# Optimization experiments

Hardware: AMD Instinct MI355X
Metric: run time of the kernel (lower is better)

Reference implementation:

```python
import jax, jax.numpy as jnp
import numpy as np

N = 100000   # nodes per graph-set
E = 600000   # edges
G = 64       # graphs in batch
H = 128      # hidden size (atom_h == voro_h == embeddings)
STEPS = 4
F_B = 90     # atom feature length
F_V = 20     # voro feature length


def setup_inputs() -> dict:
    key = jax.random.key(0)
    ks = jax.random.split(key, 16)
    inp = {
        "x_b": jax.random.uniform(ks[0], (N, F_B), dtype=jnp.float32),
        "edge_index_b": jax.random.randint(ks[1], (2, E), 0, N, dtype=jnp.int32),
        "batch_b": jnp.sort(jax.random.randint(ks[2], (N,), 0, G, dtype=jnp.int32)),
        "x_v": jax.random.uniform(ks[3], (N, F_V), dtype=jnp.float32),
        "edge_index_v": jax.random.randint(ks[4], (2, E), 0, N, dtype=jnp.int32),
        "batch_v": jnp.sort(jax.random.randint(ks[5], (N,), 0, G, dtype=jnp.int32)),
        # embedding linears (bias=False)
        "W_emb_b": jax.random.normal(ks[6], (F_B, H), dtype=jnp.float32) * 0.05,
        "W_emb_v": jax.random.normal(ks[7], (F_V, H), dtype=jnp.float32) * 0.05,
        # GatedGraphConv (the *bond* block — source applies it to both graphs)
        "ggc_weight": jax.random.normal(ks[8], (STEPS, H, H), dtype=jnp.float32) * 0.05,
        "gru_w_ih": jax.random.normal(ks[9], (3 * H, H), dtype=jnp.float32) * 0.05,
        "gru_w_hh": jax.random.normal(ks[10], (3 * H, H), dtype=jnp.float32) * 0.05,
        "gru_b_ih": jnp.zeros((3 * H,), dtype=jnp.float32),
        "gru_b_hh": jnp.zeros((3 * H,), dtype=jnp.float32),
        # output block (hidden = 2H)
        "W1": jax.random.normal(ks[11], (2 * H, 2 * H), dtype=jnp.float32) * 0.05,
        "b1": jnp.zeros((2 * H,), dtype=jnp.float32),
        "W2": jax.random.normal(ks[12], (2 * H, 1), dtype=jnp.float32) * 0.05,
        "b2": jnp.zeros((1,), dtype=jnp.float32),
    }
    return inp


def _gru_cell(m, h, w_ih, w_hh, b_ih, b_hh):
    gi = m @ w_ih.T + b_ih   # [N, 3H]
    gh = h @ w_hh.T + b_hh
    i_r, i_z, i_n = jnp.split(gi, 3, axis=-1)
    h_r, h_z, h_n = jnp.split(gh, 3, axis=-1)
    r = jax.nn.sigmoid(i_r + h_r)
    z = jax.nn.sigmoid(i_z + h_z)
    n = jnp.tanh(i_n + r * h_n)
    return (1.0 - z) * n + z * h


def _gated_graph_conv(x, edge_index, ggc_weight, gru_w_ih, gru_w_hh, gru_b_ih, gru_b_hh):
    # x: [N, H] (in_channels == out_channels, no padding needed)
    src, dst = edge_index[0], edge_index[1]
    h = x
    for i in range(STEPS):
        m = h @ ggc_weight[i]                                   # [N, H]
        agg = jax.ops.segment_sum(m[src], dst, num_segments=N)  # add-aggregation
        h = _gru_cell(agg, h, gru_w_ih, gru_w_hh, gru_b_ih, gru_b_hh)
    return h


def _mean_pool(x, batch):
    sums = jax.ops.segment_sum(x, batch, num_segments=G)
    cnt = jax.ops.segment_sum(jnp.ones((x.shape[0],), x.dtype), batch, num_segments=G)
    return sums / jnp.maximum(cnt, 1.0)[:, None]


def reference(x_b, edge_index_b, batch_b, x_v, edge_index_v, batch_v,
              W_emb_b, W_emb_v, ggc_weight, gru_w_ih, gru_w_hh, gru_b_ih, gru_b_hh,
              W1, b1, W2, b2):
    # embedding blocks: relu(linear(x)) (no bias)
    hb = jax.nn.relu(x_b @ W_emb_b)
    hv = jax.nn.relu(x_v @ W_emb_v)
    # NOTE: source (faithfully) applies mpnn_layer_bond to BOTH graphs
    hb = _gated_graph_conv(hb, edge_index_b, ggc_weight, gru_w_ih, gru_w_hh, gru_b_ih, gru_b_hh)
    hv = _gated_graph_conv(hv, edge_index_v, ggc_weight, gru_w_ih, gru_w_hh, gru_b_ih, gru_b_hh)
    gb = _mean_pool(jax.nn.relu(hb), batch_b)   # [G, H]
    gv = _mean_pool(jax.nn.relu(hv), batch_v)   # [G, H]
    g = jnp.concatenate([gb, gv], axis=1)       # [G, 2H]
    out = jax.nn.softplus(jax.nn.relu(g @ W1 + b1) @ W2 + b2)
    return out.squeeze(1)                       # [G]
```

## Files before the change

kernel.cpp:

```cpp
#include <hip/hip_runtime.h>
#include <hip/hip_bf16.h>
#include <math.h>

#define N_NODES   100000
#define N_EDGES   600000
#define NG        64
#define H         128
#define STEPS     4
#define FB        90
#define FV        20
#define NN        (2*N_NODES)
#define EE        (2*N_EDGES)
#define BSTR      40
#define NBLK      196
#define NNP       (NBLK*1024)

#define WCAT_KC   (12*64*8)
#define WCAT_HALF (8*WCAT_KC)
#define WCAT_STEP (2*WCAT_HALF)

typedef unsigned short u16;
typedef __attribute__((ext_vector_type(8))) __bf16 bf16x8;
typedef __attribute__((ext_vector_type(4))) float  floatx4;

static __device__ __forceinline__ float bf16_lo(unsigned u){ return __uint_as_float(u << 16); }
static __device__ __forceinline__ float bf16_hi(unsigned u){ return __uint_as_float(u & 0xffff0000u); }
static __device__ __forceinline__ u16 f2bf(float f){
    union { float f; unsigned u; } v; v.f = f;
    unsigned r = v.u + 0x7fffu + ((v.u >> 16) & 1u);
    return (u16)(r >> 16);
}
static __device__ __forceinline__ float fastrcp(float x){ return __builtin_amdgcn_rcpf(x); }
static __device__ __forceinline__ float fsigmoid(float x){ return fastrcp(1.f + __expf(-x)); }
static __device__ __forceinline__ float ftanh(float x){ return 1.f - 2.f*fastrcp(1.f + __expf(2.f*x)); }


__global__ void deg_kernel(const int* __restrict__ eib, const int* __restrict__ eiv,
                           int* __restrict__ deg){
    int e = blockIdx.x*blockDim.x + threadIdx.x;
    if (e >= EE) return;
    int d;
    if (e < N_EDGES) d = eib[N_EDGES + e];
    else             d = eiv[N_EDGES + (e - N_EDGES)] + N_NODES;
    atomicAdd(&deg[d], 1);
}

__global__ __launch_bounds__(256) void bsum_kernel(const int* __restrict__ deg, int* __restrict__ bsum){
    int t = threadIdx.x;
    int4 v = reinterpret_cast<const int4*>(deg)[blockIdx.x*256 + t];
    int s = v.x + v.y + v.z + v.w;
    __shared__ int ss[256];
    ss[t] = s; __syncthreads();
    for (int off = 128; off > 0; off >>= 1){ if (t < off) ss[t] += ss[t + off]; __syncthreads(); }
    if (t == 0) bsum[blockIdx.x] = ss[0];
}

__global__ __launch_bounds__(256) void bscan_kernel(const int* __restrict__ bsum, int* __restrict__ boff){
    int t = threadIdx.x;
    int v = (t < NBLK) ? bsum[t] : 0;
    __shared__ int ss[256];
    ss[t] = v; __syncthreads();
    for (int off = 1; off < 256; off <<= 1){
        int u = (t >= off) ? ss[t - off] : 0;
        __syncthreads();
        ss[t] += u;
        __syncthreads();
    }
    boff[t] = ss[t] - v;
}

__global__ __launch_bounds__(256) void scan_final_kernel(const int* __restrict__ deg, const int* __restrict__ boff,
                                                         int* __restrict__ row_ptr, int* __restrict__ cursor){
    int t = threadIdx.x, b = blockIdx.x;
    int4 v = reinterpret_cast<const int4*>(deg)[b*256 + t];
    int s = v.x + v.y + v.z + v.w;
    __shared__ int ss[256];
    ss[t] = s; __syncthreads();
    for (int off = 1; off < 256; off <<= 1){
        int u = (t >= off) ? ss[t - off] : 0;
        __syncthreads();
        ss[t] += u;
        __syncthreads();
    }
    int base = boff[b] + ss[t] - s;
    int i0 = b*1024 + t*4;
    int e0 = base, e1 = e0 + v.x, e2 = e1 + v.y, e3 = e2 + v.z;
    if (i0 < NN){
        int4 w = make_int4(e0, e1, e2, e3);
        reinterpret_cast<int4*>(row_ptr)[i0 >> 2] = w;
        reinterpret_cast<int4*>(cursor)[i0 >> 2]  = w;
    }
    if (b == 0 && t == 0) row_ptr[NN] = EE;
}

__global__ void csr_fill_kernel(const int* __restrict__ eib, const int* __restrict__ eiv,
                                int* __restrict__ cursor, int* __restrict__ csr_src){
    int e = blockIdx.x*blockDim.x + threadIdx.x;
    if (e >= EE) return;
    int s, d;
    if (e < N_EDGES){ s = eib[e];                 d = eib[N_EDGES + e]; }
    else { int e2 = e - N_EDGES; s = eiv[e2] + N_NODES; d = eiv[N_EDGES + e2] + N_NODES; }
    int pos = atomicAdd(&cursor[d], 1);
    csr_src[pos] = s;
}

__global__ __launch_bounds__(128) void fold_kernel(const float* __restrict__ ggc_w,
                                                   const float* __restrict__ w_ih,
                                                   float* __restrict__ Bfold){
    int blk = blockIdx.x;
    int s = blk >> 7, k = blk & 127;
    __shared__ float wg[128];
    int t = threadIdx.x;
    wg[t] = ggc_w[(size_t)s*H*H + (size_t)k*H + t];
    __syncthreads();
    for (int c = t; c < 384; c += 128){
        const float* wr = w_ih + (size_t)c*H;
        float acc = 0.f;
        for (int q = 0; q < 128; q += 4){
            float4 a = *reinterpret_cast<const float4*>(&wg[q]);
            float4 b = *reinterpret_cast<const float4*>(&wr[q]);
            acc += a.x*b.x + a.y*b.y + a.z*b.z + a.w*b.w;
        }
        Bfold[((size_t)s*H + k)*384 + c] = acc;
    }
}

__global__ void pack_kernel(const float* __restrict__ Bfold, const float* __restrict__ w_hh,
                            u16* __restrict__ Wcat){
    int idx = blockIdx.x*256 + threadIdx.x;
    if (idx >= STEPS*WCAT_STEP) return;
    int v    = idx & 7;
    int lane = (idx >> 3) & 63;
    int t    = (idx >> 9) % 12;
    int rem  = idx / (512*12);
    int kc   = rem & 7;
    int b1   = (rem >> 3) & 1;
    int s    = rem >> 4;
    int col16 = lane & 15, l4 = lane >> 4;
    int k = kc*32 + l4*8 + v;
    int g = t >> 2, jj = t & 3;
    int c = (4*b1 + jj)*16 + col16;
    int gc = (g == 2) ? (256 + c) : (g*128 + c);
    float val;
    if (k < 128) val = Bfold[((size_t)s*H + k)*384 + gc];
    else         val = w_hh[(size_t)gc*H + (k - 128)];
    Wcat[idx] = f2bf(val);
}


__global__ __launch_bounds__(128) void emb_kernel(const float* __restrict__ xb, const float* __restrict__ xv,
                                                  const float* __restrict__ Wb, const float* __restrict__ Wv,
                                                  u16* __restrict__ hb){
    __shared__ float xs[8][FB];
    int j = threadIdx.x;
    int n0 = blockIdx.x * 8;
    const float* x; const float* W; int K; int xoff;
    if (n0 < N_NODES){ x = xb; W = Wb; K = FB; xoff = n0; }
    else             { x = xv; W = Wv; K = FV; xoff = n0 - N_NODES; }
    for (int i = j; i < 8*K; i += 128){ int r = i / K, c = i - r*K; xs[r][c] = x[(xoff + r)*K + c]; }
    __syncthreads();
    float acc[8];
    #pragma unroll
    for (int n = 0; n < 8; ++n) acc[n] = 0.f;
    for (int k = 0; k < K; ++k){
        float w = W[k*H + j];
        #pragma unroll
        for (int n = 0; n < 8; ++n) acc[n] = fmaf(xs[n][k], w, acc[n]);
    }
    #pragma unroll
    for (int n = 0; n < 8; ++n)
        hb[(size_t)(n0 + n)*H + j] = f2bf(fmaxf(acc[n], 0.f));
}


__global__ __launch_bounds__(256) void agg_kernel(const u16* __restrict__ hb,
                                                  const int* __restrict__ row_ptr,
                                                  const int* __restrict__ csr_src,
                                                  u16* __restrict__ aggb){
    int wid  = threadIdx.x >> 6;
    int lane = threadIdx.x & 63;
    int half = lane >> 5;
    int c    = lane & 31;
    int node = blockIdx.x*4 + wid;
    int beg = row_ptr[node], end = row_ptr[node+1];
    const uint2* rows = reinterpret_cast<const uint2*>(hb);
    float s0 = 0.f, s1 = 0.f, s2 = 0.f, s3 = 0.f;
    float t0 = 0.f, t1 = 0.f, t2 = 0.f, t3 = 0.f;
    int e = beg + half;
    for (; e + 2 < end; e += 4){
        int sA = csr_src[e];
        int sB = csr_src[e + 2];
        uint2 uA = rows[(size_t)sA*32 + c];
        uint2 uB = rows[(size_t)sB*32 + c];
        s0 += bf16_lo(uA.x); s1 += bf16_hi(uA.x); s2 += bf16_lo(uA.y); s3 += bf16_hi(uA.y);
        t0 += bf16_lo(uB.x); t1 += bf16_hi(uB.x); t2 += bf16_lo(uB.y); t3 += bf16_hi(uB.y);
    }
    if (e < end){
        int sA = csr_src[e];
        uint2 uA = rows[(size_t)sA*32 + c];
        s0 += bf16_lo(uA.x); s1 += bf16_hi(uA.x); s2 += bf16_lo(uA.y); s3 += bf16_hi(uA.y);
    }
    s0 += t0; s1 += t1; s2 += t2; s3 += t3;
    s0 += __shfl_xor(s0, 32); s1 += __shfl_xor(s1, 32);
    s2 += __shfl_xor(s2, 32); s3 += __shfl_xor(s3, 32);
    if (half == 0){
        uint2 o;
        o.x = (unsigned)f2bf(s0) | ((unsigned)f2bf(s1) << 16);
        o.y = (unsigned)f2bf(s2) | ((unsigned)f2bf(s3) << 16);
        reinterpret_cast<uint2*>(aggb)[(size_t)node*32 + c] = o;
    }
}


__global__ __launch_bounds__(256, 3) void gru_mfma_kernel(const u16* __restrict__ aggb,
                                                          const u16* __restrict__ hb_in,
                                                          u16* __restrict__ hb_out,
                                                          const u16* __restrict__ Wcat,
                                                          const float* __restrict__ b_ih,
                                                          const float* __restrict__ b_hh){
    __shared__ u16 Bs[WCAT_KC];
    __shared__ u16 As[64*BSTR];
    const int t = threadIdx.x;
    const int wid = t >> 6, lane = t & 63;
    const int l15 = lane & 15, l4 = lane >> 4;
    const int n0 = blockIdx.x * 64;
    const int b1 = blockIdx.y;
    const u16* Wsrc = Wcat + (size_t)b1*WCAT_HALF;

    floatx4 accR[4], accZ[4], accNi[4], accNh[4];
    #pragma unroll
    for (int i = 0; i < 4; ++i){
        accR[i] = (floatx4){0.f,0.f,0.f,0.f};  accZ[i]  = (floatx4){0.f,0.f,0.f,0.f};
        accNi[i] = (floatx4){0.f,0.f,0.f,0.f}; accNh[i] = (floatx4){0.f,0.f,0.f,0.f};
    }

    for (int kc = 0; kc < 8; ++kc){
        __syncthreads();
        {
            const u16* src = Wsrc + (size_t)kc*WCAT_KC;
            #pragma unroll
            for (int p = 0; p < 3; ++p){
                int i = t + p*256;
                *reinterpret_cast<int4*>(&Bs[i*8]) = *reinterpret_cast<const int4*>(src + (size_t)i*8);
            }
        }
        {
            int row = t >> 2, part = t & 3;
            const u16* srcA = (kc < 4) ? aggb : hb_in;
            const int4 v = *reinterpret_cast<const int4*>(srcA + (size_t)(n0 + row)*H + (kc & 3)*32 + part*8);
            *reinterpret_cast<int4*>(&As[row*BSTR + part*8]) = v;
        }
        __syncthreads();
        bf16x8 aF = *reinterpret_cast<const bf16x8*>(&As[(wid*16 + l15)*BSTR + l4*8]);
        if (kc < 4){
            #pragma unroll
            for (int j = 0; j < 4; ++j){
                bf16x8 bR = *reinterpret_cast<const bf16x8*>(&Bs[((0*4 + j)*64 + lane)*8]);
                bf16x8 bZ = *reinterpret_cast<const bf16x8*>(&Bs[((1*4 + j)*64 + lane)*8]);
                bf16x8 bN = *reinterpret_cast<const bf16x8*>(&Bs[((2*4 + j)*64 + lane)*8]);
                accR[j]  = __builtin_amdgcn_mfma_f32_16x16x32_bf16(aF, bR, accR[j], 0, 0, 0);
                accZ[j]  = __builtin_amdgcn_mfma_f32_16x16x32_bf16(aF, bZ, accZ[j], 0, 0, 0);
                accNi[j] = __builtin_amdgcn_mfma_f32_16x16x32_bf16(aF, bN, accNi[j], 0, 0, 0);
            }
        } else {
            #pragma unroll
            for (int j = 0; j < 4; ++j){
                bf16x8 bR = *reinterpret_cast<const bf16x8*>(&Bs[((0*4 + j)*64 + lane)*8]);
                bf16x8 bZ = *reinterpret_cast<const bf16x8*>(&Bs[((1*4 + j)*64 + lane)*8]);
                bf16x8 bN = *reinterpret_cast<const bf16x8*>(&Bs[((2*4 + j)*64 + lane)*8]);
                accR[j]  = __builtin_amdgcn_mfma_f32_16x16x32_bf16(aF, bR, accR[j], 0, 0, 0);
                accZ[j]  = __builtin_amdgcn_mfma_f32_16x16x32_bf16(aF, bZ, accZ[j], 0, 0, 0);
                accNh[j] = __builtin_amdgcn_mfma_f32_16x16x32_bf16(aF, bN, accNh[j], 0, 0, 0);
            }
        }
    }

    const int rowb = n0 + wid*16 + l4*4;
    #pragma unroll
    for (int jj = 0; jj < 4; ++jj){
        int col = (4*b1 + jj)*16 + l15;
        float br  = b_ih[col]       + b_hh[col];
        float bz  = b_ih[128 + col] + b_hh[128 + col];
        float bin = b_ih[256 + col];
        float bhn = b_hh[256 + col];
        #pragma unroll
        for (int rg = 0; rg < 4; ++rg){
            int row = rowb + rg;
            float r   = fsigmoid(accR[jj][rg] + br);
            float z   = fsigmoid(accZ[jj][rg] + bz);
            float nn_ = ftanh(accNi[jj][rg] + bin + r*(accNh[jj][rg] + bhn));
            float hold = bf16_lo((unsigned)hb_in[(size_t)row*H + col]);
            float hnew = (1.f - z)*nn_ + z*hold;
            hb_out[(size_t)row*H + col] = f2bf(hnew);
        }
    }
}


__global__ __launch_bounds__(128) void pool_kernel(const u16* __restrict__ hb,
                                                   const int* __restrict__ batch_b, const int* __restrict__ batch_v,
                                                   float* __restrict__ pool){
    int j  = threadIdx.x;
    int n0 = blockIdx.x * 32;
    bool voro = (n0 >= N_NODES);
    int colbase = voro ? 128 : 0;
    int gcur = -1; float acc = 0.f;
    for (int r = 0; r < 32; ++r){
        int node = n0 + r;
        int g = voro ? batch_v[node - N_NODES] : batch_b[node];
        if (g != gcur){
            if (gcur >= 0) atomicAdd(&pool[gcur*256 + colbase + j], acc);
            acc = 0.f; gcur = g;
        }
        acc += fmaxf(bf16_lo((unsigned)hb[(size_t)node*H + j]), 0.f);
    }
    if (gcur >= 0) atomicAdd(&pool[gcur*256 + colbase + j], acc);
}

__global__ __launch_bounds__(256) void cnt_kernel(const int* __restrict__ batch_b, const int* __restrict__ batch_v,
                                                  int* __restrict__ cnt){
    __shared__ int bins[128];
    int t = threadIdx.x;
    if (t < 128) bins[t] = 0;
    __syncthreads();
    int i = blockIdx.x*256 + t;
    if (i < NN){
        int g = (i < N_NODES) ? batch_b[i] : 64 + batch_v[i - N_NODES];
        atomicAdd(&bins[g], 1);
    }
    __syncthreads();
    if (t < 128 && bins[t] > 0) atomicAdd(&cnt[t], bins[t]);
}


__global__ __launch_bounds__(256) void head_kernel(const float* __restrict__ pool, const int* __restrict__ cnt,
                                                   const float* __restrict__ W1, const float* __restrict__ b1,
                                                   const float* __restrict__ W2, const float* __restrict__ b2,
                                                   float* __restrict__ out){
    __shared__ float gs[256];
    __shared__ float wsum[4];
    int b = blockIdx.x, j = threadIdx.x;
    int c = (j < 128) ? cnt[b] : cnt[64 + b];
    float denom = (float)((c > 1) ? c : 1);
    gs[j] = pool[b*256 + j] / denom;
    __syncthreads();
    float acc = b1[j];
    for (int k = 0; k < 256; ++k) acc = fmaf(gs[k], W1[k*256 + j], acc);
    float y = fmaxf(acc, 0.f) * W2[j];
    #pragma unroll
    for (int off = 32; off > 0; off >>= 1) y += __shfl_down(y, off, 64);
    if ((j & 63) == 0) wsum[j >> 6] = y;
    __syncthreads();
    if (j == 0){
        float x = wsum[0] + wsum[1] + wsum[2] + wsum[3] + b2[0];
        float sp = (x > 0.f) ? x + log1pf(expf(-x)) : log1pf(expf(x));
        out[b] = sp;
    }
}


extern "C" void kernel_launch(void* const* d_in, const int* in_sizes, int n_in,
                              void* d_out, int out_size, void* d_ws, size_t ws_size,
                              hipStream_t stream){
    const float* x_b      = (const float*)d_in[0];
    const int*   eib      = (const int*)  d_in[1];
    const int*   batch_b  = (const int*)  d_in[2];
    const float* x_v      = (const float*)d_in[3];
    const int*   eiv      = (const int*)  d_in[4];
    const int*   batch_v  = (const int*)  d_in[5];
    const float* W_emb_b  = (const float*)d_in[6];
    const float* W_emb_v  = (const float*)d_in[7];
    const float* ggc_w    = (const float*)d_in[8];
    const float* gru_w_ih = (const float*)d_in[9];
    const float* gru_w_hh = (const float*)d_in[10];
    const float* gru_b_ih = (const float*)d_in[11];
    const float* gru_b_hh = (const float*)d_in[12];
    const float* W1       = (const float*)d_in[13];
    const float* b1       = (const float*)d_in[14];
    const float* W2       = (const float*)d_in[15];
    const float* b2       = (const float*)d_in[16];
    float* out = (float*)d_out;

    char* ws = (char*)d_ws;
    size_t off = 0;
    auto alloc = [&](size_t bytes)->char*{
        char* p = ws + off; off += (bytes + 255)/256*256; return p;
    };
    u16*   hb0      = (u16*)   alloc((size_t)NN*H*2);
    u16*   hb1      = (u16*)   alloc((size_t)NN*H*2);
    u16*   aggb     = (u16*)   alloc((size_t)NN*H*2);
    float* Bfold    = (float*) alloc((size_t)STEPS*H*384*4);
    u16*   Wcat     = (u16*)   alloc((size_t)STEPS*WCAT_STEP*2);
    int*   row_ptr  = (int*)   alloc((size_t)(NN+1)*4);
    int*   deg      = (int*)   alloc((size_t)NNP*4);
    int*   cursor   = (int*)   alloc((size_t)NN*4);
    int*   csr_src  = (int*)   alloc((size_t)EE*4);
    int*   bsum     = (int*)   alloc((size_t)256*4);
    int*   boff     = (int*)   alloc((size_t)256*4);
    float* pool     = (float*) alloc((size_t)NG*2*H*4);
    int*   cnt      = (int*)   alloc((size_t)2*NG*4);
    (void)ws_size; (void)in_sizes; (void)n_in; (void)out_size;

    hipMemsetAsync(deg,  0, (size_t)NNP*4, stream);
    hipMemsetAsync(pool, 0, (size_t)NG*2*H*4, stream);
    hipMemsetAsync(cnt,  0, (size_t)2*NG*4, stream);

    deg_kernel        <<<(EE + 255)/256, 256, 0, stream>>>(eib, eiv, deg);
    bsum_kernel       <<<NBLK, 256, 0, stream>>>(deg, bsum);
    bscan_kernel      <<<1, 256, 0, stream>>>(bsum, boff);
    scan_final_kernel <<<NBLK, 256, 0, stream>>>(deg, boff, row_ptr, cursor);
    csr_fill_kernel   <<<(EE + 255)/256, 256, 0, stream>>>(eib, eiv, cursor, csr_src);
    fold_kernel       <<<STEPS*H, 128, 0, stream>>>(ggc_w, gru_w_ih, Bfold);
    pack_kernel       <<<(STEPS*WCAT_STEP + 255)/256, 256, 0, stream>>>(Bfold, gru_w_hh, Wcat);

    emb_kernel<<<NN/8, 128, 0, stream>>>(x_b, x_v, W_emb_b, W_emb_v, hb0);

    u16* hbs[2] = { hb0, hb1 };
    for (int s = 0; s < STEPS; ++s){
        u16* hin  = hbs[s & 1];
        u16* hout = hbs[(s + 1) & 1];
        agg_kernel     <<<NN/4, 256, 0, stream>>>(hin, row_ptr, csr_src, aggb);
        gru_mfma_kernel<<<dim3(NN/64, 2), 256, 0, stream>>>(aggb, hin, hout,
                                                            Wcat + (size_t)s*WCAT_STEP,
                                                            gru_b_ih, gru_b_hh);
    }

    pool_kernel<<<NN/32, 128, 0, stream>>>(hb0, batch_b, batch_v, pool);
    cnt_kernel <<<(NN + 255)/256, 256, 0, stream>>>(batch_b, batch_v, cnt);
    head_kernel<<<NG, 256, 0, stream>>>(pool, cnt, W1, b1, W2, b2, out);
}
```

Measured before the change: 937.1 us.

## Build CSR via two-level bucket sort and widen aggregation gathers to 16 bytes

Replaces the single-pass atomic CSR fill with a two-stage bucketed sort. Edges are first appended into 64-node buckets using per-bucket global atomics, with the blocks partitioned by bucket group. Each bucket is then scattered into csr_src using shared-memory atomics, aiming to cut contended global atomics and make the scattered writes more local. Separately, the aggregation kernel now gathers 16-byte rows with four edge lanes per node instead of two, which needs an extra shuffle-reduction stage; the new CSR build also adds two kernels and an extra buffer.

```diff
diff --git a/kernel.cpp b/kernel.cpp
--- a/kernel.cpp
+++ b/kernel.cpp
@@ -14,6 +14,7 @@
 #define BSTR      40
 #define NBLK      196
 #define NNP       (NBLK*1024)
+#define NBUCK     (NN/64)
 
 #define WCAT_KC   (12*64*8)
 #define WCAT_HALF (8*WCAT_KC)
@@ -70,7 +71,7 @@
 }
 
 __global__ __launch_bounds__(256) void scan_final_kernel(const int* __restrict__ deg, const int* __restrict__ boff,
-                                                         int* __restrict__ row_ptr, int* __restrict__ cursor){
+                                                         int* __restrict__ row_ptr){
     int t = threadIdx.x, b = blockIdx.x;
     int4 v = reinterpret_cast<const int4*>(deg)[b*256 + t];
     int s = v.x + v.y + v.z + v.w;
@@ -86,22 +87,48 @@
     int i0 = b*1024 + t*4;
     int e0 = base, e1 = e0 + v.x, e2 = e1 + v.y, e3 = e2 + v.z;
     if (i0 < NN){
-        int4 w = make_int4(e0, e1, e2, e3);
-        reinterpret_cast<int4*>(row_ptr)[i0 >> 2] = w;
-        reinterpret_cast<int4*>(cursor)[i0 >> 2]  = w;
+        reinterpret_cast<int4*>(row_ptr)[i0 >> 2] = make_int4(e0, e1, e2, e3);
     }
     if (b == 0 && t == 0) row_ptr[NN] = EE;
 }
 
-__global__ void csr_fill_kernel(const int* __restrict__ eib, const int* __restrict__ eiv,
-                                int* __restrict__ cursor, int* __restrict__ csr_src){
-    int e = blockIdx.x*blockDim.x + threadIdx.x;
-    if (e >= EE) return;
-    int s, d;
-    if (e < N_EDGES){ s = eib[e];                 d = eib[N_EDGES + e]; }
-    else { int e2 = e - N_EDGES; s = eiv[e2] + N_NODES; d = eiv[N_EDGES + e2] + N_NODES; }
-    int pos = atomicAdd(&cursor[d], 1);
-    csr_src[pos] = s;
+__global__ void bcur_init_kernel(const int* __restrict__ row_ptr, int* __restrict__ bcur){
+    int b = blockIdx.x*blockDim.x + threadIdx.x;
+    if (b < NBUCK) bcur[b] = row_ptr[b*64];
+}
+
+__global__ __launch_bounds__(256) void bucket_fill_kernel(const int* __restrict__ eib, const int* __restrict__ eiv,
+                                                          int* __restrict__ bcur, int* __restrict__ bucket_buf){
+    int g   = blockIdx.x & 7;
+    int bid = blockIdx.x >> 3;
+    int nb  = gridDim.x >> 3;
+    for (int e = bid*256 + threadIdx.x; e < EE; e += nb*256){
+        int s, d;
+        if (e < N_EDGES){ s = eib[e];                 d = eib[N_EDGES + e]; }
+        else { int e2 = e - N_EDGES; s = eiv[e2] + N_NODES; d = eiv[N_EDGES + e2] + N_NODES; }
+        int b = d >> 6;
+        if ((b & 7) == g){
+            int pos = atomicAdd(&bcur[b], 1);
+            bucket_buf[pos] = (s << 6) | (d & 63);
+        }
+    }
+}
+
+__global__ __launch_bounds__(256) void bucket_scatter_kernel(const int* __restrict__ bucket_buf,
+                                                             const int* __restrict__ row_ptr,
+                                                             int* __restrict__ csr_src){
+    __shared__ int cur[64];
+    int b = blockIdx.x, t = threadIdx.x;
+    int base = row_ptr[b*64];
+    int cnt  = row_ptr[b*64 + 64] - base;
+    if (t < 64) cur[t] = row_ptr[b*64 + t];
+    __syncthreads();
+    for (int i = t; i < cnt; i += 256){
+        int entry = bucket_buf[base + i];
+        int d = entry & 63, s = entry >> 6;
+        int pos = atomicAdd(&cur[d], 1);
+        csr_src[pos] = s;
+    }
 }
 
 __global__ __launch_bounds__(128) void fold_kernel(const float* __restrict__ ggc_w,
@@ -179,35 +206,42 @@
                                                   u16* __restrict__ aggb){
     int wid  = threadIdx.x >> 6;
     int lane = threadIdx.x & 63;
-    int half = lane >> 5;
-    int c    = lane & 31;
+    int q    = lane >> 4;
+    int c    = lane & 15;
     int node = blockIdx.x*4 + wid;
     int beg = row_ptr[node], end = row_ptr[node+1];
-    const uint2* rows = reinterpret_cast<const uint2*>(hb);
-    float s0 = 0.f, s1 = 0.f, s2 = 0.f, s3 = 0.f;
-    float t0 = 0.f, t1 = 0.f, t2 = 0.f, t3 = 0.f;
-    int e = beg + half;
-    for (; e + 2 < end; e += 4){
+    const uint4* rows = reinterpret_cast<const uint4*>(hb);
+    float s0=0.f,s1=0.f,s2=0.f,s3=0.f,s4=0.f,s5=0.f,s6=0.f,s7=0.f;
+    float u0=0.f,u1=0.f,u2=0.f,u3=0.f,u4=0.f,u5=0.f,u6=0.f,u7=0.f;
+    int e = beg + q;
+    for (; e + 4 < end; e += 8){
         int sA = csr_src[e];
-        int sB = csr_src[e + 2];
-        uint2 uA = rows[(size_t)sA*32 + c];
-        uint2 uB = rows[(size_t)sB*32 + c];
-        s0 += bf16_lo(uA.x); s1 += bf16_hi(uA.x); s2 += bf16_lo(uA.y); s3 += bf16_hi(uA.y);
-        t0 += bf16_lo(uB.x); t1 += bf16_hi(uB.x); t2 += bf16_lo(uB.y); t3 += bf16_hi(uB.y);
+        int sB = csr_src[e + 4];
+        uint4 a = rows[(size_t)sA*16 + c];
+        uint4 b = rows[(size_t)sB*16 + c];
+        s0 += bf16_lo(a.x); s1 += bf16_hi(a.x); s2 += bf16_lo(a.y); s3 += bf16_hi(a.y);
+        s4 += bf16_lo(a.z); s5 += bf16_hi(a.z); s6 += bf16_lo(a.w); s7 += bf16_hi(a.w);
+        u0 += bf16_lo(b.x); u1 += bf16_hi(b.x); u2 += bf16_lo(b.y); u3 += bf16_hi(b.y);
+        u4 += bf16_lo(b.z); u5 += bf16_hi(b.z); u6 += bf16_lo(b.w); u7 += bf16_hi(b.w);
     }
     if (e < end){
         int sA = csr_src[e];
-        uint2 uA = rows[(size_t)sA*32 + c];
-        s0 += bf16_lo(uA.x); s1 += bf16_hi(uA.x); s2 += bf16_lo(uA.y); s3 += bf16_hi(uA.y);
-    }
-    s0 += t0; s1 += t1; s2 += t2; s3 += t3;
-    s0 += __shfl_xor(s0, 32); s1 += __shfl_xor(s1, 32);
-    s2 += __shfl_xor(s2, 32); s3 += __shfl_xor(s3, 32);
-    if (half == 0){
-        uint2 o;
+        uint4 a = rows[(size_t)sA*16 + c];
+        s0 += bf16_lo(a.x); s1 += bf16_hi(a.x); s2 += bf16_lo(a.y); s3 += bf16_hi(a.y);
+        s4 += bf16_lo(a.z); s5 += bf16_hi(a.z); s6 += bf16_lo(a.w); s7 += bf16_hi(a.w);
+    }
+    s0 += u0; s1 += u1; s2 += u2; s3 += u3; s4 += u4; s5 += u5; s6 += u6; s7 += u7;
+    s0 += __shfl_xor(s0, 16); s1 += __shfl_xor(s1, 16); s2 += __shfl_xor(s2, 16); s3 += __shfl_xor(s3, 16);
+    s4 += __shfl_xor(s4, 16); s5 += __shfl_xor(s5, 16); s6 += __shfl_xor(s6, 16); s7 += __shfl_xor(s7, 16);
+    s0 += __shfl_xor(s0, 32); s1 += __shfl_xor(s1, 32); s2 += __shfl_xor(s2, 32); s3 += __shfl_xor(s3, 32);
+    s4 += __shfl_xor(s4, 32); s5 += __shfl_xor(s5, 32); s6 += __shfl_xor(s6, 32); s7 += __shfl_xor(s7, 32);
+    if (q == 0){
+        uint4 o;
         o.x = (unsigned)f2bf(s0) | ((unsigned)f2bf(s1) << 16);
         o.y = (unsigned)f2bf(s2) | ((unsigned)f2bf(s3) << 16);
-        reinterpret_cast<uint2*>(aggb)[(size_t)node*32 + c] = o;
+        o.z = (unsigned)f2bf(s4) | ((unsigned)f2bf(s5) << 16);
+        o.w = (unsigned)f2bf(s6) | ((unsigned)f2bf(s7) << 16);
+        reinterpret_cast<uint4*>(aggb)[(size_t)node*16 + c] = o;
     }
 }
 
@@ -393,8 +427,9 @@
     u16*   Wcat     = (u16*)   alloc((size_t)STEPS*WCAT_STEP*2);
     int*   row_ptr  = (int*)   alloc((size_t)(NN+1)*4);
     int*   deg      = (int*)   alloc((size_t)NNP*4);
-    int*   cursor   = (int*)   alloc((size_t)NN*4);
     int*   csr_src  = (int*)   alloc((size_t)EE*4);
+    int*   bucket_buf = (int*) alloc((size_t)EE*4);
+    int*   bcur     = (int*)   alloc((size_t)NBUCK*4);
     int*   bsum     = (int*)   alloc((size_t)256*4);
     int*   boff     = (int*)   alloc((size_t)256*4);
     float* pool     = (float*) alloc((size_t)NG*2*H*4);
@@ -405,13 +440,15 @@
     hipMemsetAsync(pool, 0, (size_t)NG*2*H*4, stream);
     hipMemsetAsync(cnt,  0, (size_t)2*NG*4, stream);
 
-    deg_kernel        <<<(EE + 255)/256, 256, 0, stream>>>(eib, eiv, deg);
-    bsum_kernel       <<<NBLK, 256, 0, stream>>>(deg, bsum);
-    bscan_kernel      <<<1, 256, 0, stream>>>(bsum, boff);
-    scan_final_kernel <<<NBLK, 256, 0, stream>>>(deg, boff, row_ptr, cursor);
-    csr_fill_kernel   <<<(EE + 255)/256, 256, 0, stream>>>(eib, eiv, cursor, csr_src);
-    fold_kernel       <<<STEPS*H, 128, 0, stream>>>(ggc_w, gru_w_ih, Bfold);
-    pack_kernel       <<<(STEPS*WCAT_STEP + 255)/256, 256, 0, stream>>>(Bfold, gru_w_hh, Wcat);
+    deg_kernel           <<<(EE + 255)/256, 256, 0, stream>>>(eib, eiv, deg);
+    bsum_kernel          <<<NBLK, 256, 0, stream>>>(deg, bsum);
+    bscan_kernel         <<<1, 256, 0, stream>>>(bsum, boff);
+    scan_final_kernel    <<<NBLK, 256, 0, stream>>>(deg, boff, row_ptr);
+    bcur_init_kernel     <<<(NBUCK + 255)/256, 256, 0, stream>>>(row_ptr, bcur);
+    bucket_fill_kernel   <<<2048, 256, 0, stream>>>(eib, eiv, bcur, bucket_buf);
+    bucket_scatter_kernel<<<NBUCK, 256, 0, stream>>>(bucket_buf, row_ptr, csr_src);
+    fold_kernel          <<<STEPS*H, 128, 0, stream>>>(ggc_w, gru_w_ih, Bfold);
+    pack_kernel          <<<(STEPS*WCAT_STEP + 255)/256, 256, 0, stream>>>(Bfold, gru_w_hh, Wcat);
 
     emb_kernel<<<NN/8, 128, 0, stream>>>(x_b, x_v, W_emb_b, W_emb_v, hb0);
 
```

Result: slower. 1.069 ms (+14.0%).
